# Optimization experiments

Measured on AMD Instinct MI355X. Metric: run time of the kernel, lower is better.

Reference implementation:

```python
import jax, jax.numpy as jnp
import numpy as np

B, C, H, W = 16, 512, 32, 32
HW = H * W  # == input_features == output_features for shapes to be consistent


def setup_inputs() -> dict:
    key = jax.random.key(0)
    k1, k2, k3 = jax.random.split(key, 3)
    node1 = jax.random.normal(k1, (B, C, H, W), dtype=jnp.float32)
    node2 = jax.random.normal(k2, (B, C, H, W), dtype=jnp.float32)
    # nn.Linear(input_features, output_features, bias=False).weight: [out, in]
    W_c = jax.random.normal(k3, (HW, HW), dtype=jnp.float32) * (1.0 / np.sqrt(HW))
    return {"node1": node1, "node2": node2, "W_c": W_c}


def reference(node1, node2, W_c):
    b, c, h, w = node1.shape
    hw = h * w
    n1 = node1.reshape(b, c, hw)  # [B, C, HW]
    n2 = node2.reshape(b, c, hw)  # [B, C, HW]
    # x = W_c(n1): Linear applies y = x @ W^T  -> [B, C, HW_out]
    x = jnp.einsum('bch,oh->bco', n1, W_c)
    # e = bmm(x.permute(0,2,1), n2): [B, HW_out, C] @ [B, C, HW] -> [B, HW_out, HW]
    e = jnp.einsum('bco,bch->boh', x, n2)
    a = jax.nn.softmax(e, axis=-1)  # softmax over last dim (HW of node2)
    # m = bmm(n2, a): [B, C, HW] @ [B, HW, HW] -> [B, C, HW]
    m = jnp.einsum('bck,bkj->bcj', n2, a)
    return m
```

## Files before the change

### kernel.cpp

```cpp
#include <hip/hip_runtime.h>
#include <math.h>


typedef _Float16 f16;
typedef _Float16 f16x8 __attribute__((ext_vector_type(8)));
typedef _Float16 f16x4 __attribute__((ext_vector_type(4)));
typedef float f32x4 __attribute__((ext_vector_type(4)));

#define L2E 1.442695040888963f

#define WG_BARRIER() asm volatile("s_waitcnt lgkmcnt(0)\ns_barrier" ::: "memory")

__global__ __launch_bounds__(256) void prep(const float* __restrict__ n1,
                                            const float* __restrict__ Wc,
                                            const float* __restrict__ n2,
                                            f16* __restrict__ n1f, f16* __restrict__ Wf,
                                            f16* __restrict__ n2f, f16* __restrict__ n2t) {
    const int bid = blockIdx.x, tid = threadIdx.x;
    if (bid < 4608) {
        const float* s = (bid < 4096) ? n1 : Wc;
        f16* d = (bid < 4096) ? n1f : Wf;
        const size_t i = ((size_t)(bid < 4096 ? bid : bid - 4096) * 256 + tid) * 8;
        f32x4 a = *(const f32x4*)(s + i);
        f32x4 b = *(const f32x4*)(s + i + 4);
        f16x8 o;
        o[0] = (f16)a[0]; o[1] = (f16)a[1]; o[2] = (f16)a[2]; o[3] = (f16)a[3];
        o[4] = (f16)b[0]; o[5] = (f16)b[1]; o[6] = (f16)b[2]; o[7] = (f16)b[3];
        *(f16x8*)(d + i) = o;
        return;
    }
    const int id = bid - 4608;
    const int b = id >> 7;
    const int ry = (id & 127) >> 4;
    const int cx = id & 15;
    const float* S = n2 + (size_t)b * 512 * 1024;
    f16* Dn = n2f + (size_t)b * 512 * 1024;
    f16* Dt = n2t + (size_t)b * 1024 * 512;
    __shared__ f16 Ts[64 * 72];
    const int r0 = ry * 64, c0 = cx * 64;
    const int rr = tid >> 3, cc8 = (tid & 7) * 8;
#pragma unroll
    for (int h = 0; h < 2; ++h) {
        const int row = r0 + rr + 32 * h;
        const float* s = S + (size_t)row * 1024 + c0 + cc8;
        f32x4 a = *(const f32x4*)s, bq = *(const f32x4*)(s + 4);
        f16x8 o;
        o[0] = (f16)a[0]; o[1] = (f16)a[1]; o[2] = (f16)a[2]; o[3] = (f16)a[3];
        o[4] = (f16)bq[0]; o[5] = (f16)bq[1]; o[6] = (f16)bq[2]; o[7] = (f16)bq[3];
        *(f16x8*)&Ts[(rr + 32 * h) * 72 + cc8] = o;
        *(f16x8*)(Dn + (size_t)row * 1024 + c0 + cc8) = o;
    }
    __syncthreads();
    const int j = tid >> 2, k16 = (tid & 3) * 16;
    f16* d = Dt + (size_t)(c0 + j) * 512 + r0 + k16;
    f16x8 o0, o1;
#pragma unroll
    for (int i = 0; i < 8; ++i) {
        o0[i] = Ts[(k16 + i) * 72 + j];
        o1[i] = Ts[(k16 + 8 + i) * 72 + j];
    }
    *(f16x8*)d = o0;
    *(f16x8*)(d + 8) = o1;
}

__global__ __launch_bounds__(256) void stats_partial(const f16* __restrict__ Et,
                                                     float* __restrict__ Pm,
                                                     float* __restrict__ Ps) {
    const int b = blockIdx.x & 15, chunk = blockIdx.x >> 4;
    const int half = threadIdx.x >> 7;
    const int t = threadIdx.x & 127;
    const f16* p = Et + (size_t)b * 1024 * 1024 +
                   ((size_t)chunk * 64 + half * 32) * 1024 + t * 8;
    float m[8], s[8];
#pragma unroll
    for (int c = 0; c < 8; ++c) { m[c] = -3.0e38f; s[c] = 0.f; }
#pragma unroll 4
    for (int j = 0; j < 32; ++j) {
        f16x8 v8 = *(const f16x8*)(p + (size_t)j * 1024);
#pragma unroll
        for (int c = 0; c < 8; ++c) {
            float v = (float)v8[c];
            float nm = fmaxf(m[c], v);
            s[c] = s[c] * __expf(m[c] - nm) + __expf(v - nm);
            m[c] = nm;
        }
    }
    const int idx32 = b * 32 + chunk * 2 + half;
    f32x4 mo0, mo1, so0, so1;
#pragma unroll
    for (int c = 0; c < 4; ++c) { mo0[c] = m[c]; mo1[c] = m[c + 4];
                                  so0[c] = s[c]; so1[c] = s[c + 4]; }
    float* pmo = Pm + (size_t)idx32 * 1024 + t * 8;
    float* pso = Ps + (size_t)idx32 * 1024 + t * 8;
    *(f32x4*)pmo = mo0; *(f32x4*)(pmo + 4) = mo1;
    *(f32x4*)pso = so0; *(f32x4*)(pso + 4) = so1;
}

__global__ __launch_bounds__(256) void stats_combine(const float* __restrict__ Pm,
                                                     const float* __restrict__ Ps,
                                                     float* __restrict__ Sc) {
    const int g = blockIdx.x * 256 + threadIdx.x;
    const int b = g >> 10, o = g & 1023;
    const float* pm = Pm + (size_t)b * 32 * 1024 + o;
    const float* ps = Ps + (size_t)b * 32 * 1024 + o;
    float M = -3.0e38f;
#pragma unroll
    for (int c = 0; c < 32; ++c) M = fmaxf(M, pm[c * 1024]);
    float S = 0.f;
#pragma unroll
    for (int c = 0; c < 32; ++c) S += ps[c * 1024] * __expf(pm[c * 1024] - M);
    Sc[g] = (M + __logf(S)) * L2E;
}

__device__ __forceinline__ f16x8 expb(f16x8 b, f32x4 cl, f32x4 ch) {
    f16x8 t;
#pragma unroll
    for (int i = 0; i < 4; ++i) t[i] = (f16)exp2f(fmaf((float)b[i], L2E, -cl[i]));
#pragma unroll
    for (int i = 0; i < 4; ++i) t[4 + i] = (f16)exp2f(fmaf((float)b[4 + i], L2E, -ch[i]));
    return t;
}

template <int NS, bool EXPB>
__device__ __forceinline__ void gemm_core(const char* gA0, const char* gA1,
                                          const char* gB, const float* gSp,
                                          char* SM, int sOff, int wm, int wn,
                                          int col, int swz16, f32x4 (&acc)[4][4]) {
    f16x8 a00 = *(const f16x8*)gA0, a01 = *(const f16x8*)gA1;
    f16x8 b0 = *(const f16x8*)gB;
    f32x4 c00, c01, c10, c11;
    if (EXPB) { c00 = *(const f32x4*)gSp; c01 = *(const f32x4*)(gSp + 4); }
    {
        char* dA = SM + sOff;
        *(f16x8*)dA = a00;
        *(f16x8*)(dA + 8192) = a01;
        char* dB = SM + 32768 + sOff;
        *(f16x8*)dB = EXPB ? expb(b0, c00, c01) : b0;
    }
    f16x8 a10 = *(const f16x8*)(gA0 + 64), a11 = *(const f16x8*)(gA1 + 64);
    f16x8 b1 = *(const f16x8*)(gB + 64);
    if (EXPB) { c10 = *(const f32x4*)(gSp + 32); c11 = *(const f32x4*)(gSp + 36); }
    a00 = *(const f16x8*)(gA0 + 128); a01 = *(const f16x8*)(gA1 + 128);
    b0 = *(const f16x8*)(gB + 128);
    if (EXPB) { c00 = *(const f32x4*)(gSp + 64); c01 = *(const f32x4*)(gSp + 68); }
    WG_BARRIER();
#pragma unroll
    for (int kb = 0; kb < NS; ++kb) {
        const char* Ac = SM + (kb & 1) * 16384;
        const char* Bc = SM + 32768 + (kb & 1) * 8192;
        f16x8 fa[4], fb[4];
#pragma unroll
        for (int u = 0; u < 4; ++u)
            fa[u] = *(const f16x8*)(Ac + (wm + u * 16 + col) * 64 + swz16);
#pragma unroll
        for (int v = 0; v < 4; ++v)
            fb[v] = *(const f16x8*)(Bc + (wn + v * 16 + col) * 64 + swz16);
#pragma unroll
        for (int u = 0; u < 4; ++u)
#pragma unroll
            for (int v = 0; v < 4; ++v)
                acc[u][v] = __builtin_amdgcn_mfma_f32_16x16x32_f16(fa[u], fb[v],
                                                                   acc[u][v], 0, 0, 0);
        if (kb + 1 < NS) {
            char* dA = SM + ((kb + 1) & 1) * 16384 + sOff;
            char* dB = SM + 32768 + ((kb + 1) & 1) * 8192 + sOff;
            if ((kb & 1) == 0) {
                *(f16x8*)dA = a10;
                *(f16x8*)(dA + 8192) = a11;
                *(f16x8*)dB = EXPB ? expb(b1, c10, c11) : b1;
                if (kb + 3 < NS) {
                    a10 = *(const f16x8*)(gA0 + (size_t)(kb + 3) * 64);
                    a11 = *(const f16x8*)(gA1 + (size_t)(kb + 3) * 64);
                    b1 = *(const f16x8*)(gB + (size_t)(kb + 3) * 64);
                    if (EXPB) {
                        c10 = *(const f32x4*)(gSp + (size_t)(kb + 3) * 32);
                        c11 = *(const f32x4*)(gSp + (size_t)(kb + 3) * 32 + 4);
                    }
                }
            } else {
                *(f16x8*)dA = a00;
                *(f16x8*)(dA + 8192) = a01;
                *(f16x8*)dB = EXPB ? expb(b0, c00, c01) : b0;
                if (kb + 3 < NS) {
                    a00 = *(const f16x8*)(gA0 + (size_t)(kb + 3) * 64);
                    a01 = *(const f16x8*)(gA1 + (size_t)(kb + 3) * 64);
                    b0 = *(const f16x8*)(gB + (size_t)(kb + 3) * 64);
                    if (EXPB) {
                        c00 = *(const f32x4*)(gSp + (size_t)(kb + 3) * 32);
                        c01 = *(const f32x4*)(gSp + (size_t)(kb + 3) * 32 + 4);
                    }
                }
            }
            WG_BARRIER();
        }
    }
}

__device__ __forceinline__ void epilogue_tr(f32x4 (&acc)[4][4], char* SM, f16* dst0,
                                            int dstRow, int m0, int n0, int tid) {
    const int lane = tid & 63, wave = tid >> 6;
    const int col = lane & 15, quad = lane >> 4;
    const int wn = (wave >> 2) * 64;
    const int mh_w = (wave >> 1) & 1;
    const int wm_loc = (wave & 1) * 64;
    const int j = tid >> 2, seg = (tid & 3) * 32;
    WG_BARRIER();
    f16* Tt = (f16*)SM;
#pragma unroll
    for (int mh = 0; mh < 2; ++mh) {
        if (mh_w == mh) {
#pragma unroll
            for (int u = 0; u < 4; ++u)
#pragma unroll
                for (int v = 0; v < 4; ++v) {
                    f16x4 p;
#pragma unroll
                    for (int r = 0; r < 4; ++r) p[r] = (f16)acc[u][v][r];
                    *(f16x4*)&Tt[(wn + v * 16 + col) * 136 + wm_loc + u * 16 + quad * 4] = p;
                }
        }
        WG_BARRIER();
        f16* dst = dst0 + (size_t)(n0 + j) * dstRow + m0 + mh * 128 + seg;
#pragma unroll
        for (int c8 = 0; c8 < 32; c8 += 8)
            *(f16x8*)(dst + c8) = *(const f16x8*)&Tt[j * 136 + seg + c8];
        if (mh == 0) WG_BARRIER();
    }
}

__global__ __launch_bounds__(512) void gemm1_nt_xt(const f16* __restrict__ A,
                                                   const f16* __restrict__ Bw,
                                                   f16* __restrict__ Xt) {
    const int K = 1024;
    const int id = blockIdx.x;
    const int xcd = id & 7, loc = id >> 3;
    const int b = xcd * 2 + (loc >> 4);
    const int m0 = ((loc >> 3) & 1) * 256;
    const int n0 = (loc & 7) * 128;
    A += (size_t)b * 512 * K;
    Xt += (size_t)b * 1024 * 512;
    __shared__ __attribute__((aligned(16))) char SM[49152];
    const int tid = threadIdx.x, lane = tid & 63, wave = tid >> 6;
    const int col = lane & 15, quad = lane >> 4;
    const int wm = (wave & 3) * 64, wn = (wave >> 2) * 64;
    const int srow = tid >> 2, sslot = tid & 3;
    const int sOff = srow * 64 + ((sslot ^ ((srow >> 1) & 3)) * 16);
    const int swz16 = (quad ^ ((col >> 1) & 3)) * 16;
    const char* gA0 = (const char*)A + (size_t)(m0 + srow) * K * 2 + sslot * 16;
    const char* gA1 = gA0 + (size_t)128 * K * 2;
    const char* gB = (const char*)Bw + (size_t)(n0 + srow) * K * 2 + sslot * 16;
    f32x4 acc[4][4] = {};
    gemm_core<32, false>(gA0, gA1, gB, nullptr, SM, sOff, wm, wn, col, swz16, acc);
    epilogue_tr(acc, SM, Xt, 512, m0, n0, tid);
}

__global__ __launch_bounds__(512) void gemm2_nt_et(const f16* __restrict__ A,
                                                   const f16* __restrict__ B,
                                                   f16* __restrict__ Et) {
    const int K = 512;
    const int id = blockIdx.x;
    const int xcd = id & 7, loc = id >> 3;
    const int b = xcd * 2 + (loc >> 5);
    const int m0 = ((loc >> 3) & 3) * 256;
    const int n0 = (loc & 7) * 128;
    A += (size_t)b * 1024 * K;
    B += (size_t)b * 1024 * K;
    Et += (size_t)b * 1024 * 1024;
    __shared__ __attribute__((aligned(16))) char SM[49152];
    const int tid = threadIdx.x, lane = tid & 63, wave = tid >> 6;
    const int col = lane & 15, quad = lane >> 4;
    const int wm = (wave & 3) * 64, wn = (wave >> 2) * 64;
    const int srow = tid >> 2, sslot = tid & 3;
    const int sOff = srow * 64 + ((sslot ^ ((srow >> 1) & 3)) * 16);
    const int swz16 = (quad ^ ((col >> 1) & 3)) * 16;
    const char* gA0 = (const char*)A + (size_t)(m0 + srow) * K * 2 + sslot * 16;
    const char* gA1 = gA0 + (size_t)128 * K * 2;
    const char* gB = (const char*)B + (size_t)(n0 + srow) * K * 2 + sslot * 16;
    f32x4 acc[4][4] = {};
    gemm_core<16, false>(gA0, gA1, gB, nullptr, SM, sOff, wm, wn, col, swz16, acc);
    epilogue_tr(acc, SM, Et, 1024, m0, n0, tid);
}

__global__ __launch_bounds__(512) void gemm3_nt_out(const f16* __restrict__ A,
                                                    const f16* __restrict__ Et,
                                                    const float* __restrict__ Sc,
                                                    float* __restrict__ C) {
    const int K = 1024;
    const int id = blockIdx.x;
    const int xcd = id & 7, loc = id >> 3;
    const int b = xcd * 2 + (loc >> 4);
    const int m0 = ((loc >> 3) & 1) * 256;
    const int n0 = (loc & 7) * 128;
    A += (size_t)b * 512 * K;
    Et += (size_t)b * 1024 * K;
    Sc += (size_t)b * 1024;
    C += (size_t)b * 512 * 1024;
    __shared__ __attribute__((aligned(16))) char SM[49152];
    const int tid = threadIdx.x, lane = tid & 63, wave = tid >> 6;
    const int col = lane & 15, quad = lane >> 4;
    const int wm = (wave & 3) * 64, wn = (wave >> 2) * 64;
    const int srow = tid >> 2, sslot = tid & 3;
    const int sOff = srow * 64 + ((sslot ^ ((srow >> 1) & 3)) * 16);
    const int swz16 = (quad ^ ((col >> 1) & 3)) * 16;
    const char* gA0 = (const char*)A + (size_t)(m0 + srow) * K * 2 + sslot * 16;
    const char* gA1 = gA0 + (size_t)128 * K * 2;
    const char* gB = (const char*)Et + (size_t)(n0 + srow) * K * 2 + sslot * 16;
    const float* gSp = Sc + sslot * 8;
    f32x4 acc[4][4] = {};
    gemm_core<32, true>(gA0, gA1, gB, gSp, SM, sOff, wm, wn, col, swz16, acc);

#pragma unroll
    for (int u = 0; u < 4; ++u)
#pragma unroll
        for (int v = 0; v < 4; ++v)
#pragma unroll
            for (int r = 0; r < 4; ++r)
                C[(size_t)(m0 + wm + u * 16 + quad * 4 + r) * 1024 + n0 + wn + v * 16 + col] =
                    acc[u][v][r];
}

extern "C" void kernel_launch(void* const* d_in, const int* in_sizes, int n_in,
                              void* d_out, int out_size, void* d_ws, size_t ws_size,
                              hipStream_t stream) {
    const float* n1 = (const float*)d_in[0];
    const float* n2 = (const float*)d_in[1];
    const float* Wc = (const float*)d_in[2];
    float* out = (float*)d_out;
    char* ws = (char*)d_ws;

    f16* n2t = (f16*)(ws);
    f16* Xt  = (f16*)(ws + (16u << 20));
    f16* Wf  = (f16*)(ws + (32u << 20));
    f16* Et  = (f16*)(ws + (32u << 20));
    f16* n1f = (f16*)(ws + (64u << 20));
    f16* n2f = (f16*)(ws + (80u << 20));
    float* Pm = (float*)(ws + (64u << 20));
    float* Ps = (float*)(ws + (66u << 20));
    float* Sc = (float*)(ws + (68u << 20));

    prep<<<6656, dim3(256), 0, stream>>>(n1, Wc, n2, n1f, Wf, n2f, n2t);
    gemm1_nt_xt<<<256, dim3(512), 0, stream>>>(n1f, Wf, Xt);
    gemm2_nt_et<<<512, dim3(512), 0, stream>>>(Xt, n2t, Et);
    stats_partial<<<256, dim3(256), 0, stream>>>(Et, Pm, Ps);
    stats_combine<<<64, dim3(256), 0, stream>>>(Pm, Ps, Sc);
    gemm3_nt_out<<<256, dim3(512), 0, stream>>>(n2f, Et, Sc, out);
}
```

Measured before the change: 205.1 us.

## Fuse softmax row stats into gemm2 epilogue and shrink GEMM tiles to 128x128

Removes the separate stats_partial kernel: gemm2 now computes per-row max and sum-of-exp partials from its accumulators with wave shuffles and writes them out. stats_combine reduces 16 partials per row instead of 32 and works in base-2. All three GEMMs move from 256x128 tiles with 512 threads to 128x128 tiles with 256 threads and smaller LDS, doubling the grid size. The fusion avoids a full extra read of the E matrix. The smaller tiles add occupancy but lower data reuse per block.

```diff
diff --git a/kernel.cpp b/kernel.cpp
--- a/kernel.cpp
+++ b/kernel.cpp
@@ -63,53 +63,21 @@
     *(f16x8*)(d + 8) = o1;
 }
 
-__global__ __launch_bounds__(256) void stats_partial(const f16* __restrict__ Et,
-                                                     float* __restrict__ Pm,
-                                                     float* __restrict__ Ps) {
-    const int b = blockIdx.x & 15, chunk = blockIdx.x >> 4;
-    const int half = threadIdx.x >> 7;
-    const int t = threadIdx.x & 127;
-    const f16* p = Et + (size_t)b * 1024 * 1024 +
-                   ((size_t)chunk * 64 + half * 32) * 1024 + t * 8;
-    float m[8], s[8];
-#pragma unroll
-    for (int c = 0; c < 8; ++c) { m[c] = -3.0e38f; s[c] = 0.f; }
-#pragma unroll 4
-    for (int j = 0; j < 32; ++j) {
-        f16x8 v8 = *(const f16x8*)(p + (size_t)j * 1024);
-#pragma unroll
-        for (int c = 0; c < 8; ++c) {
-            float v = (float)v8[c];
-            float nm = fmaxf(m[c], v);
-            s[c] = s[c] * __expf(m[c] - nm) + __expf(v - nm);
-            m[c] = nm;
-        }
-    }
-    const int idx32 = b * 32 + chunk * 2 + half;
-    f32x4 mo0, mo1, so0, so1;
-#pragma unroll
-    for (int c = 0; c < 4; ++c) { mo0[c] = m[c]; mo1[c] = m[c + 4];
-                                  so0[c] = s[c]; so1[c] = s[c + 4]; }
-    float* pmo = Pm + (size_t)idx32 * 1024 + t * 8;
-    float* pso = Ps + (size_t)idx32 * 1024 + t * 8;
-    *(f32x4*)pmo = mo0; *(f32x4*)(pmo + 4) = mo1;
-    *(f32x4*)pso = so0; *(f32x4*)(pso + 4) = so1;
-}
-
 __global__ __launch_bounds__(256) void stats_combine(const float* __restrict__ Pm,
                                                      const float* __restrict__ Ps,
                                                      float* __restrict__ Sc) {
     const int g = blockIdx.x * 256 + threadIdx.x;
     const int b = g >> 10, o = g & 1023;
-    const float* pm = Pm + (size_t)b * 32 * 1024 + o;
-    const float* ps = Ps + (size_t)b * 32 * 1024 + o;
+    const int mt = o >> 7, ml = o & 127;
+    const float* pm = Pm + ((size_t)(b * 8 + mt) * 16) * 128 + ml;
+    const float* ps = Ps + ((size_t)(b * 8 + mt) * 16) * 128 + ml;
     float M = -3.0e38f;
 #pragma unroll
-    for (int c = 0; c < 32; ++c) M = fmaxf(M, pm[c * 1024]);
+    for (int p = 0; p < 16; ++p) M = fmaxf(M, pm[p * 128]);
     float S = 0.f;
 #pragma unroll
-    for (int c = 0; c < 32; ++c) S += ps[c * 1024] * __expf(pm[c * 1024] - M);
-    Sc[g] = (M + __logf(S)) * L2E;
+    for (int p = 0; p < 16; ++p) S += ps[p * 128] * exp2f(pm[p * 128] - M);
+    Sc[g] = M + __log2f(S);
 }
 
 __device__ __forceinline__ f16x8 expb(f16x8 b, f32x4 cl, f32x4 ch) {
@@ -122,32 +90,39 @@
 }
 
 template <int NS, bool EXPB>
-__device__ __forceinline__ void gemm_core(const char* gA0, const char* gA1,
-                                          const char* gB, const float* gSp,
-                                          char* SM, int sOff, int wm, int wn,
-                                          int col, int swz16, f32x4 (&acc)[4][4]) {
-    f16x8 a00 = *(const f16x8*)gA0, a01 = *(const f16x8*)gA1;
-    f16x8 b0 = *(const f16x8*)gB;
-    f32x4 c00, c01, c10, c11;
-    if (EXPB) { c00 = *(const f32x4*)gSp; c01 = *(const f32x4*)(gSp + 4); }
-    {
-        char* dA = SM + sOff;
-        *(f16x8*)dA = a00;
-        *(f16x8*)(dA + 8192) = a01;
-        char* dB = SM + 32768 + sOff;
-        *(f16x8*)dB = EXPB ? expb(b0, c00, c01) : b0;
-    }
-    f16x8 a10 = *(const f16x8*)(gA0 + 64), a11 = *(const f16x8*)(gA1 + 64);
-    f16x8 b1 = *(const f16x8*)(gB + 64);
-    if (EXPB) { c10 = *(const f32x4*)(gSp + 32); c11 = *(const f32x4*)(gSp + 36); }
-    a00 = *(const f16x8*)(gA0 + 128); a01 = *(const f16x8*)(gA1 + 128);
-    b0 = *(const f16x8*)(gB + 128);
-    if (EXPB) { c00 = *(const f32x4*)(gSp + 64); c01 = *(const f32x4*)(gSp + 68); }
+__device__ __forceinline__ void gemm_core128(const char* gA, const char* gB,
+                                             const float* gS, char* SM,
+                                             int sOff0, int sOff1,
+                                             int wm, int wn, int col, int swz16,
+                                             f32x4 (&acc)[4][4]) {
+    f32x4 c0a, c0b, c0c, c0d, c1a, c1b, c1c, c1d;
+    f16x8 pa0 = *(const f16x8*)gA, pa1 = *(const f16x8*)(gA + 16);
+    f16x8 pb0 = *(const f16x8*)gB, pb1 = *(const f16x8*)(gB + 16);
+    if (EXPB) {
+        c0a = *(const f32x4*)gS;        c0b = *(const f32x4*)(gS + 4);
+        c0c = *(const f32x4*)(gS + 8);  c0d = *(const f32x4*)(gS + 12);
+    }
+    *(f16x8*)(SM + sOff0) = pa0;
+    *(f16x8*)(SM + sOff1) = pa1;
+    *(f16x8*)(SM + 16384 + sOff0) = EXPB ? expb(pb0, c0a, c0b) : pb0;
+    *(f16x8*)(SM + 16384 + sOff1) = EXPB ? expb(pb1, c0c, c0d) : pb1;
+    f16x8 qa0 = *(const f16x8*)(gA + 64), qa1 = *(const f16x8*)(gA + 80);
+    f16x8 qb0 = *(const f16x8*)(gB + 64), qb1 = *(const f16x8*)(gB + 80);
+    if (EXPB) {
+        c1a = *(const f32x4*)(gS + 32); c1b = *(const f32x4*)(gS + 36);
+        c1c = *(const f32x4*)(gS + 40); c1d = *(const f32x4*)(gS + 44);
+    }
+    pa0 = *(const f16x8*)(gA + 128); pa1 = *(const f16x8*)(gA + 144);
+    pb0 = *(const f16x8*)(gB + 128); pb1 = *(const f16x8*)(gB + 144);
+    if (EXPB) {
+        c0a = *(const f32x4*)(gS + 64); c0b = *(const f32x4*)(gS + 68);
+        c0c = *(const f32x4*)(gS + 72); c0d = *(const f32x4*)(gS + 76);
+    }
     WG_BARRIER();
 #pragma unroll
     for (int kb = 0; kb < NS; ++kb) {
-        const char* Ac = SM + (kb & 1) * 16384;
-        const char* Bc = SM + 32768 + (kb & 1) * 8192;
+        const char* Ac = SM + (kb & 1) * 8192;
+        const char* Bc = SM + 16384 + (kb & 1) * 8192;
         f16x8 fa[4], fb[4];
 #pragma unroll
         for (int u = 0; u < 4; ++u)
@@ -162,32 +137,40 @@
                 acc[u][v] = __builtin_amdgcn_mfma_f32_16x16x32_f16(fa[u], fb[v],
                                                                    acc[u][v], 0, 0, 0);
         if (kb + 1 < NS) {
-            char* dA = SM + ((kb + 1) & 1) * 16384 + sOff;
-            char* dB = SM + 32768 + ((kb + 1) & 1) * 8192 + sOff;
+            char* dA = SM + ((kb + 1) & 1) * 8192;
+            char* dB = SM + 16384 + ((kb + 1) & 1) * 8192;
             if ((kb & 1) == 0) {
-                *(f16x8*)dA = a10;
-                *(f16x8*)(dA + 8192) = a11;
-                *(f16x8*)dB = EXPB ? expb(b1, c10, c11) : b1;
+                *(f16x8*)(dA + sOff0) = qa0;
+                *(f16x8*)(dA + sOff1) = qa1;
+                *(f16x8*)(dB + sOff0) = EXPB ? expb(qb0, c1a, c1b) : qb0;
+                *(f16x8*)(dB + sOff1) = EXPB ? expb(qb1, c1c, c1d) : qb1;
                 if (kb + 3 < NS) {
-                    a10 = *(const f16x8*)(gA0 + (size_t)(kb + 3) * 64);
-                    a11 = *(const f16x8*)(gA1 + (size_t)(kb + 3) * 64);
-                    b1 = *(const f16x8*)(gB + (size_t)(kb + 3) * 64);
+                    qa0 = *(const f16x8*)(gA + (size_t)(kb + 3) * 64);
+                    qa1 = *(const f16x8*)(gA + (size_t)(kb + 3) * 64 + 16);
+                    qb0 = *(const f16x8*)(gB + (size_t)(kb + 3) * 64);
+                    qb1 = *(const f16x8*)(gB + (size_t)(kb + 3) * 64 + 16);
                     if (EXPB) {
-                        c10 = *(const f32x4*)(gSp + (size_t)(kb + 3) * 32);
-                        c11 = *(const f32x4*)(gSp + (size_t)(kb + 3) * 32 + 4);
+                        c1a = *(const f32x4*)(gS + (size_t)(kb + 3) * 32);
+                        c1b = *(const f32x4*)(gS + (size_t)(kb + 3) * 32 + 4);
+                        c1c = *(const f32x4*)(gS + (size_t)(kb + 3) * 32 + 8);
+                        c1d = *(const f32x4*)(gS + (size_t)(kb + 3) * 32 + 12);
                     }
                 }
             } else {
-                *(f16x8*)dA = a00;
-                *(f16x8*)(dA + 8192) = a01;
-                *(f16x8*)dB = EXPB ? expb(b0, c00, c01) : b0;
+                *(f16x8*)(dA + sOff0) = pa0;
+                *(f16x8*)(dA + sOff1) = pa1;
+                *(f16x8*)(dB + sOff0) = EXPB ? expb(pb0, c0a, c0b) : pb0;
+                *(f16x8*)(dB + sOff1) = EXPB ? expb(pb1, c0c, c0d) : pb1;
                 if (kb + 3 < NS) {
-                    a00 = *(const f16x8*)(gA0 + (size_t)(kb + 3) * 64);
-                    a01 = *(const f16x8*)(gA1 + (size_t)(kb + 3) * 64);
-                    b0 = *(const f16x8*)(gB + (size_t)(kb + 3) * 64);
+                    pa0 = *(const f16x8*)(gA + (size_t)(kb + 3) * 64);
+                    pa1 = *(const f16x8*)(gA + (size_t)(kb + 3) * 64 + 16);
+                    pb0 = *(const f16x8*)(gB + (size_t)(kb + 3) * 64);
+                    pb1 = *(const f16x8*)(gB + (size_t)(kb + 3) * 64 + 16);
                     if (EXPB) {
-                        c00 = *(const f32x4*)(gSp + (size_t)(kb + 3) * 32);
-                        c01 = *(const f32x4*)(gSp + (size_t)(kb + 3) * 32 + 4);
+                        c0a = *(const f32x4*)(gS + (size_t)(kb + 3) * 32);
+                        c0b = *(const f32x4*)(gS + (size_t)(kb + 3) * 32 + 4);
+                        c0c = *(const f32x4*)(gS + (size_t)(kb + 3) * 32 + 8);
+                        c0d = *(const f32x4*)(gS + (size_t)(kb + 3) * 32 + 12);
                     }
                 }
             }
@@ -196,118 +179,156 @@
     }
 }
 
-__device__ __forceinline__ void epilogue_tr(f32x4 (&acc)[4][4], char* SM, f16* dst0,
-                                            int dstRow, int m0, int n0, int tid) {
+__device__ __forceinline__ void epilogue_tr128(f32x4 (&acc)[4][4], char* SM,
+                                               f16* dst0, int dstRow, int m0,
+                                               int n0, int tid) {
     const int lane = tid & 63, wave = tid >> 6;
     const int col = lane & 15, quad = lane >> 4;
-    const int wn = (wave >> 2) * 64;
-    const int mh_w = (wave >> 1) & 1;
-    const int wm_loc = (wave & 1) * 64;
-    const int j = tid >> 2, seg = (tid & 3) * 32;
+    const int wm = ((wave >> 1) & 1) * 64, wn = (wave & 1) * 64;
     WG_BARRIER();
     f16* Tt = (f16*)SM;
 #pragma unroll
-    for (int mh = 0; mh < 2; ++mh) {
-        if (mh_w == mh) {
-#pragma unroll
-            for (int u = 0; u < 4; ++u)
-#pragma unroll
-                for (int v = 0; v < 4; ++v) {
-                    f16x4 p;
-#pragma unroll
-                    for (int r = 0; r < 4; ++r) p[r] = (f16)acc[u][v][r];
-                    *(f16x4*)&Tt[(wn + v * 16 + col) * 136 + wm_loc + u * 16 + quad * 4] = p;
-                }
+    for (int u = 0; u < 4; ++u)
+#pragma unroll
+        for (int v = 0; v < 4; ++v) {
+            f16x4 p;
+#pragma unroll
+            for (int r = 0; r < 4; ++r) p[r] = (f16)acc[u][v][r];
+            *(f16x4*)&Tt[(wn + v * 16 + col) * 136 + wm + u * 16 + quad * 4] = p;
         }
-        WG_BARRIER();
-        f16* dst = dst0 + (size_t)(n0 + j) * dstRow + m0 + mh * 128 + seg;
-#pragma unroll
-        for (int c8 = 0; c8 < 32; c8 += 8)
-            *(f16x8*)(dst + c8) = *(const f16x8*)&Tt[j * 136 + seg + c8];
-        if (mh == 0) WG_BARRIER();
-    }
-}
-
-__global__ __launch_bounds__(512) void gemm1_nt_xt(const f16* __restrict__ A,
+    WG_BARRIER();
+    const int j = tid >> 1, seg = (tid & 1) * 64;
+    f16* dst = dst0 + (size_t)(n0 + j) * dstRow + m0 + seg;
+#pragma unroll
+    for (int c8 = 0; c8 < 64; c8 += 8)
+        *(f16x8*)(dst + c8) = *(const f16x8*)&Tt[j * 136 + seg + c8];
+}
+
+__global__ __launch_bounds__(256) void gemm1_nt_xt(const f16* __restrict__ A,
                                                    const f16* __restrict__ Bw,
                                                    f16* __restrict__ Xt) {
     const int K = 1024;
     const int id = blockIdx.x;
     const int xcd = id & 7, loc = id >> 3;
-    const int b = xcd * 2 + (loc >> 4);
-    const int m0 = ((loc >> 3) & 1) * 256;
+    const int b = xcd * 2 + (loc >> 5);
+    const int m0 = ((loc >> 3) & 3) * 128;
     const int n0 = (loc & 7) * 128;
     A += (size_t)b * 512 * K;
     Xt += (size_t)b * 1024 * 512;
-    __shared__ __attribute__((aligned(16))) char SM[49152];
+    __shared__ __attribute__((aligned(16))) char SM[34816];
     const int tid = threadIdx.x, lane = tid & 63, wave = tid >> 6;
     const int col = lane & 15, quad = lane >> 4;
-    const int wm = (wave & 3) * 64, wn = (wave >> 2) * 64;
-    const int srow = tid >> 2, sslot = tid & 3;
-    const int sOff = srow * 64 + ((sslot ^ ((srow >> 1) & 3)) * 16);
+    const int wm = ((wave >> 1) & 1) * 64, wn = (wave & 1) * 64;
+    const int srow = tid >> 1, spair = (tid & 1) * 2;
+    const int sx = (srow >> 1) & 3;
+    const int sOff0 = srow * 64 + ((spair ^ sx) * 16);
+    const int sOff1 = srow * 64 + (((spair + 1) ^ sx) * 16);
     const int swz16 = (quad ^ ((col >> 1) & 3)) * 16;
-    const char* gA0 = (const char*)A + (size_t)(m0 + srow) * K * 2 + sslot * 16;
-    const char* gA1 = gA0 + (size_t)128 * K * 2;
-    const char* gB = (const char*)Bw + (size_t)(n0 + srow) * K * 2 + sslot * 16;
+    const char* gA = (const char*)A + (size_t)(m0 + srow) * K * 2 + spair * 16;
+    const char* gB = (const char*)Bw + (size_t)(n0 + srow) * K * 2 + spair * 16;
     f32x4 acc[4][4] = {};
-    gemm_core<32, false>(gA0, gA1, gB, nullptr, SM, sOff, wm, wn, col, swz16, acc);
-    epilogue_tr(acc, SM, Xt, 512, m0, n0, tid);
-}
-
-__global__ __launch_bounds__(512) void gemm2_nt_et(const f16* __restrict__ A,
+    gemm_core128<32, false>(gA, gB, nullptr, SM, sOff0, sOff1, wm, wn, col, swz16, acc);
+    epilogue_tr128(acc, SM, Xt, 512, m0, n0, tid);
+}
+
+__global__ __launch_bounds__(256) void gemm2_nt_et(const f16* __restrict__ A,
                                                    const f16* __restrict__ B,
-                                                   f16* __restrict__ Et) {
+                                                   f16* __restrict__ Et,
+                                                   float* __restrict__ Pm,
+                                                   float* __restrict__ Ps) {
     const int K = 512;
     const int id = blockIdx.x;
     const int xcd = id & 7, loc = id >> 3;
-    const int b = xcd * 2 + (loc >> 5);
-    const int m0 = ((loc >> 3) & 3) * 256;
+    const int b = xcd * 2 + (loc >> 6);
+    const int m0 = ((loc >> 3) & 7) * 128;
     const int n0 = (loc & 7) * 128;
     A += (size_t)b * 1024 * K;
     B += (size_t)b * 1024 * K;
     Et += (size_t)b * 1024 * 1024;
-    __shared__ __attribute__((aligned(16))) char SM[49152];
+    __shared__ __attribute__((aligned(16))) char SM[34816];
     const int tid = threadIdx.x, lane = tid & 63, wave = tid >> 6;
     const int col = lane & 15, quad = lane >> 4;
-    const int wm = (wave & 3) * 64, wn = (wave >> 2) * 64;
-    const int srow = tid >> 2, sslot = tid & 3;
-    const int sOff = srow * 64 + ((sslot ^ ((srow >> 1) & 3)) * 16);
+    const int wm = ((wave >> 1) & 1) * 64, wn = (wave & 1) * 64;
+    const int srow = tid >> 1, spair = (tid & 1) * 2;
+    const int sx = (srow >> 1) & 3;
+    const int sOff0 = srow * 64 + ((spair ^ sx) * 16);
+    const int sOff1 = srow * 64 + (((spair + 1) ^ sx) * 16);
     const int swz16 = (quad ^ ((col >> 1) & 3)) * 16;
-    const char* gA0 = (const char*)A + (size_t)(m0 + srow) * K * 2 + sslot * 16;
-    const char* gA1 = gA0 + (size_t)128 * K * 2;
-    const char* gB = (const char*)B + (size_t)(n0 + srow) * K * 2 + sslot * 16;
+    const char* gA = (const char*)A + (size_t)(m0 + srow) * K * 2 + spair * 16;
+    const char* gB = (const char*)B + (size_t)(n0 + srow) * K * 2 + spair * 16;
     f32x4 acc[4][4] = {};
-    gemm_core<16, false>(gA0, gA1, gB, nullptr, SM, sOff, wm, wn, col, swz16, acc);
-    epilogue_tr(acc, SM, Et, 1024, m0, n0, tid);
-}
-
-__global__ __launch_bounds__(512) void gemm3_nt_out(const f16* __restrict__ A,
+    gemm_core128<16, false>(gA, gB, nullptr, SM, sOff0, sOff1, wm, wn, col, swz16, acc);
+
+    {
+        float pm[16], ps[16];
+#pragma unroll
+        for (int u = 0; u < 4; ++u)
+#pragma unroll
+            for (int r = 0; r < 4; ++r) {
+                float w0 = (float)(f16)acc[u][0][r] * L2E;
+                float w1 = (float)(f16)acc[u][1][r] * L2E;
+                float w2 = (float)(f16)acc[u][2][r] * L2E;
+                float w3 = (float)(f16)acc[u][3][r] * L2E;
+                float m2 = fmaxf(fmaxf(w0, w1), fmaxf(w2, w3));
+                float s = exp2f(w0 - m2) + exp2f(w1 - m2) +
+                          exp2f(w2 - m2) + exp2f(w3 - m2);
+                pm[u * 4 + r] = m2;
+                ps[u * 4 + r] = s;
+            }
+#pragma unroll
+        for (int d = 1; d < 16; d <<= 1)
+#pragma unroll
+            for (int i = 0; i < 16; ++i) {
+                float om = __shfl_xor(pm[i], d, 64);
+                float os = __shfl_xor(ps[i], d, 64);
+                float nm = fmaxf(pm[i], om);
+                ps[i] = ps[i] * exp2f(pm[i] - nm) + os * exp2f(om - nm);
+                pm[i] = nm;
+            }
+        if (col == 0) {
+            const int part = ((b * 8 + (m0 >> 7)) * 8 + (n0 >> 7)) * 2 + (wave & 1);
+            float* bm = Pm + (size_t)part * 128;
+            float* bs = Ps + (size_t)part * 128;
+#pragma unroll
+            for (int i = 0; i < 16; ++i) {
+                const int ml = wm + (i >> 2) * 16 + quad * 4 + (i & 3);
+                bm[ml] = pm[i];
+                bs[ml] = ps[i];
+            }
+        }
+    }
+
+    epilogue_tr128(acc, SM, Et, 1024, m0, n0, tid);
+}
+
+__global__ __launch_bounds__(256) void gemm3_nt_out(const f16* __restrict__ A,
                                                     const f16* __restrict__ Et,
                                                     const float* __restrict__ Sc,
                                                     float* __restrict__ C) {
     const int K = 1024;
     const int id = blockIdx.x;
     const int xcd = id & 7, loc = id >> 3;
-    const int b = xcd * 2 + (loc >> 4);
-    const int m0 = ((loc >> 3) & 1) * 256;
+    const int b = xcd * 2 + (loc >> 5);
+    const int m0 = ((loc >> 3) & 3) * 128;
     const int n0 = (loc & 7) * 128;
     A += (size_t)b * 512 * K;
     Et += (size_t)b * 1024 * K;
     Sc += (size_t)b * 1024;
     C += (size_t)b * 512 * 1024;
-    __shared__ __attribute__((aligned(16))) char SM[49152];
+    __shared__ __attribute__((aligned(16))) char SM[34816];
     const int tid = threadIdx.x, lane = tid & 63, wave = tid >> 6;
     const int col = lane & 15, quad = lane >> 4;
-    const int wm = (wave & 3) * 64, wn = (wave >> 2) * 64;
-    const int srow = tid >> 2, sslot = tid & 3;
-    const int sOff = srow * 64 + ((sslot ^ ((srow >> 1) & 3)) * 16);
+    const int wm = ((wave >> 1) & 1) * 64, wn = (wave & 1) * 64;
+    const int srow = tid >> 1, spair = (tid & 1) * 2;
+    const int sx = (srow >> 1) & 3;
+    const int sOff0 = srow * 64 + ((spair ^ sx) * 16);
+    const int sOff1 = srow * 64 + (((spair + 1) ^ sx) * 16);
     const int swz16 = (quad ^ ((col >> 1) & 3)) * 16;
-    const char* gA0 = (const char*)A + (size_t)(m0 + srow) * K * 2 + sslot * 16;
-    const char* gA1 = gA0 + (size_t)128 * K * 2;
-    const char* gB = (const char*)Et + (size_t)(n0 + srow) * K * 2 + sslot * 16;
-    const float* gSp = Sc + sslot * 8;
+    const char* gA = (const char*)A + (size_t)(m0 + srow) * K * 2 + spair * 16;
+    const char* gB = (const char*)Et + (size_t)(n0 + srow) * K * 2 + spair * 16;
+    const float* gS = Sc + spair * 8;
     f32x4 acc[4][4] = {};
-    gemm_core<32, true>(gA0, gA1, gB, gSp, SM, sOff, wm, wn, col, swz16, acc);
+    gemm_core128<32, true>(gA, gB, gS, SM, sOff0, sOff1, wm, wn, col, swz16, acc);
 
 #pragma unroll
     for (int u = 0; u < 4; ++u)
@@ -335,13 +356,12 @@
     f16* n1f = (f16*)(ws + (64u << 20));
     f16* n2f = (f16*)(ws + (80u << 20));
     float* Pm = (float*)(ws + (64u << 20));
-    float* Ps = (float*)(ws + (66u << 20));
-    float* Sc = (float*)(ws + (68u << 20));
+    float* Ps = (float*)(ws + (65u << 20));
+    float* Sc = (float*)(ws + (66u << 20));
 
     prep<<<6656, dim3(256), 0, stream>>>(n1, Wc, n2, n1f, Wf, n2f, n2t);
-    gemm1_nt_xt<<<256, dim3(512), 0, stream>>>(n1f, Wf, Xt);
-    gemm2_nt_et<<<512, dim3(512), 0, stream>>>(Xt, n2t, Et);
-    stats_partial<<<256, dim3(256), 0, stream>>>(Et, Pm, Ps);
+    gemm1_nt_xt<<<512, dim3(256), 0, stream>>>(n1f, Wf, Xt);
+    gemm2_nt_et<<<1024, dim3(256), 0, stream>>>(Xt, n2t, Et, Pm, Ps);
     stats_combine<<<64, dim3(256), 0, stream>>>(Pm, Ps, Sc);
-    gemm3_nt_out<<<256, dim3(512), 0, stream>>>(n2f, Et, Sc, out);
-}
+    gemm3_nt_out<<<512, dim3(256), 0, stream>>>(n2f, Et, Sc, out);
+}
```

Result: slower. 233.8 us (+14.0%).

## Fuse softmax partial max/sum stats into gemm2 epilogue, drop stats_partial kernel

Applied to the files above, without the earlier changes.

The per-column online max/sum softmax statistics are now computed from the gemm2 accumulators in registers, reduced across lanes with xor shuffles, and written as partial results per tile half. This removes the stats_partial kernel, which re-read the full 32 MB f16 energy matrix, along with its launch. stats_combine now merges 16 partials per column in the base-2 domain. The cost is more register pressure and shuffle work in the gemm2 epilogue.

```diff
diff --git a/kernel.cpp b/kernel.cpp
--- a/kernel.cpp
+++ b/kernel.cpp
@@ -63,53 +63,21 @@
     *(f16x8*)(d + 8) = o1;
 }
 
-__global__ __launch_bounds__(256) void stats_partial(const f16* __restrict__ Et,
-                                                     float* __restrict__ Pm,
-                                                     float* __restrict__ Ps) {
-    const int b = blockIdx.x & 15, chunk = blockIdx.x >> 4;
-    const int half = threadIdx.x >> 7;
-    const int t = threadIdx.x & 127;
-    const f16* p = Et + (size_t)b * 1024 * 1024 +
-                   ((size_t)chunk * 64 + half * 32) * 1024 + t * 8;
-    float m[8], s[8];
-#pragma unroll
-    for (int c = 0; c < 8; ++c) { m[c] = -3.0e38f; s[c] = 0.f; }
-#pragma unroll 4
-    for (int j = 0; j < 32; ++j) {
-        f16x8 v8 = *(const f16x8*)(p + (size_t)j * 1024);
-#pragma unroll
-        for (int c = 0; c < 8; ++c) {
-            float v = (float)v8[c];
-            float nm = fmaxf(m[c], v);
-            s[c] = s[c] * __expf(m[c] - nm) + __expf(v - nm);
-            m[c] = nm;
-        }
-    }
-    const int idx32 = b * 32 + chunk * 2 + half;
-    f32x4 mo0, mo1, so0, so1;
-#pragma unroll
-    for (int c = 0; c < 4; ++c) { mo0[c] = m[c]; mo1[c] = m[c + 4];
-                                  so0[c] = s[c]; so1[c] = s[c + 4]; }
-    float* pmo = Pm + (size_t)idx32 * 1024 + t * 8;
-    float* pso = Ps + (size_t)idx32 * 1024 + t * 8;
-    *(f32x4*)pmo = mo0; *(f32x4*)(pmo + 4) = mo1;
-    *(f32x4*)pso = so0; *(f32x4*)(pso + 4) = so1;
-}
-
 __global__ __launch_bounds__(256) void stats_combine(const float* __restrict__ Pm,
                                                      const float* __restrict__ Ps,
                                                      float* __restrict__ Sc) {
     const int g = blockIdx.x * 256 + threadIdx.x;
     const int b = g >> 10, o = g & 1023;
-    const float* pm = Pm + (size_t)b * 32 * 1024 + o;
-    const float* ps = Ps + (size_t)b * 32 * 1024 + o;
+    const int mt = o >> 8, ml = o & 255;
+    const float* pm = Pm + ((size_t)(b * 4 + mt) * 16) * 256 + ml;
+    const float* ps = Ps + ((size_t)(b * 4 + mt) * 16) * 256 + ml;
     float M = -3.0e38f;
 #pragma unroll
-    for (int c = 0; c < 32; ++c) M = fmaxf(M, pm[c * 1024]);
+    for (int p = 0; p < 16; ++p) M = fmaxf(M, pm[p * 256]);
     float S = 0.f;
 #pragma unroll
-    for (int c = 0; c < 32; ++c) S += ps[c * 1024] * __expf(pm[c * 1024] - M);
-    Sc[g] = (M + __logf(S)) * L2E;
+    for (int p = 0; p < 16; ++p) S += ps[p * 256] * exp2f(pm[p * 256] - M);
+    Sc[g] = M + __log2f(S);
 }
 
 __device__ __forceinline__ f16x8 expb(f16x8 b, f32x4 cl, f32x4 ch) {
@@ -256,7 +224,9 @@
 
 __global__ __launch_bounds__(512) void gemm2_nt_et(const f16* __restrict__ A,
                                                    const f16* __restrict__ B,
-                                                   f16* __restrict__ Et) {
+                                                   f16* __restrict__ Et,
+                                                   float* __restrict__ Pm,
+                                                   float* __restrict__ Ps) {
     const int K = 512;
     const int id = blockIdx.x;
     const int xcd = id & 7, loc = id >> 3;
@@ -278,6 +248,47 @@
     const char* gB = (const char*)B + (size_t)(n0 + srow) * K * 2 + sslot * 16;
     f32x4 acc[4][4] = {};
     gemm_core<16, false>(gA0, gA1, gB, nullptr, SM, sOff, wm, wn, col, swz16, acc);
+
+    {
+        float pm[16], ps[16];
+#pragma unroll
+        for (int u = 0; u < 4; ++u)
+#pragma unroll
+            for (int r = 0; r < 4; ++r) {
+                float w0 = (float)(f16)acc[u][0][r] * L2E;
+                float w1 = (float)(f16)acc[u][1][r] * L2E;
+                float w2 = (float)(f16)acc[u][2][r] * L2E;
+                float w3 = (float)(f16)acc[u][3][r] * L2E;
+                float m2 = fmaxf(fmaxf(w0, w1), fmaxf(w2, w3));
+                float s = exp2f(w0 - m2) + exp2f(w1 - m2) +
+                          exp2f(w2 - m2) + exp2f(w3 - m2);
+                pm[u * 4 + r] = m2;
+                ps[u * 4 + r] = s;
+            }
+#pragma unroll
+        for (int d = 1; d < 16; d <<= 1)
+#pragma unroll
+            for (int i = 0; i < 16; ++i) {
+                float om = __shfl_xor(pm[i], d, 64);
+                float os = __shfl_xor(ps[i], d, 64);
+                float nm = fmaxf(pm[i], om);
+                ps[i] = ps[i] * exp2f(pm[i] - nm) + os * exp2f(om - nm);
+                pm[i] = nm;
+            }
+        if (col == 0) {
+            const int part = ((b * 4 + (m0 >> 8)) * 8 + (n0 >> 7)) * 2 + (wave >> 2);
+            float* bm = Pm + (size_t)part * 256;
+            float* bs = Ps + (size_t)part * 256;
+            const int wmq = (wave & 3) * 64 + quad * 4;
+#pragma unroll
+            for (int i = 0; i < 16; ++i) {
+                const int ml = wmq + (i >> 2) * 16 + (i & 3);
+                bm[ml] = pm[i];
+                bs[ml] = ps[i];
+            }
+        }
+    }
+
     epilogue_tr(acc, SM, Et, 1024, m0, n0, tid);
 }
 
@@ -335,13 +346,12 @@
     f16* n1f = (f16*)(ws + (64u << 20));
     f16* n2f = (f16*)(ws + (80u << 20));
     float* Pm = (float*)(ws + (64u << 20));
-    float* Ps = (float*)(ws + (66u << 20));
-    float* Sc = (float*)(ws + (68u << 20));
+    float* Ps = (float*)(ws + (65u << 20));
+    float* Sc = (float*)(ws + (66u << 20));
 
     prep<<<6656, dim3(256), 0, stream>>>(n1, Wc, n2, n1f, Wf, n2f, n2t);
     gemm1_nt_xt<<<256, dim3(512), 0, stream>>>(n1f, Wf, Xt);
-    gemm2_nt_et<<<512, dim3(512), 0, stream>>>(Xt, n2t, Et);
-    stats_partial<<<256, dim3(256), 0, stream>>>(Et, Pm, Ps);
+    gemm2_nt_et<<<512, dim3(512), 0, stream>>>(Xt, n2t, Et, Pm, Ps);
     stats_combine<<<64, dim3(256), 0, stream>>>(Pm, Ps, Sc);
     gemm3_nt_out<<<256, dim3(512), 0, stream>>>(n2f, Et, Sc, out);
 }
```

Result: slower. 216.5 us (+5.6%).
